# Performance work log

Hardware: AMD Instinct MI355X
Metric: run time of the kernel (lower is better)

The kernel has to match this reference:

```python
import jax, jax.numpy as jnp
import numpy as np

E, T, H, I = 32, 512, 2048, 768


def setup_inputs() -> dict:
    key = jax.random.key(0)
    k1, k2, k3, k4 = jax.random.split(key, 4)
    scale = 1.0 / np.sqrt(H)
    return {
        "routed_input": jax.random.normal(k1, (E, T, H), dtype=jnp.float32),
        "gate_proj": jax.random.normal(k2, (E, I, H), dtype=jnp.float32) * scale,
        "up_proj": jax.random.normal(k3, (E, I, H), dtype=jnp.float32) * scale,
        "down_proj": jax.random.normal(k4, (E, H, I), dtype=jnp.float32) * scale,
    }


def reference(routed_input, gate_proj, up_proj, down_proj):
    # routed_input: [E, T, H]; per-expert SwiGLU MLP, concat over experts.
    gate = jnp.einsum("eth,eih->eti", routed_input, gate_proj)
    up = jnp.einsum("eth,eih->eti", routed_input, up_proj)
    hidden = jax.nn.silu(gate) * up  # [E, T, I]
    out = jnp.einsum("eti,ehi->eth", hidden, down_proj)  # [E, T, H]
    return out.reshape(E * T, H)
```

## Files before the change

### kernel.cpp

```cpp
#include <hip/hip_runtime.h>


#define NE 32
#define NT 512
#define NH 2048
#define NI 768

typedef short        short8  __attribute__((ext_vector_type(8)));
typedef float        floatx4 __attribute__((ext_vector_type(4)));
typedef unsigned int uintx4  __attribute__((ext_vector_type(4)));
typedef __attribute__((address_space(1))) const unsigned int g_u32;
typedef __attribute__((address_space(3))) unsigned int l_u32;

__device__ __forceinline__ void gl_lds16(const void* g, void* l) {
    __builtin_amdgcn_global_load_lds((g_u32*)g, (l_u32*)l, 16, 0, 0);
}

__device__ __forceinline__ unsigned int cvt_pk_bf16(float lo, float hi) {
    unsigned int r;
    asm("v_cvt_pk_bf16_f32 %0, %1, %2" : "=v"(r) : "v"(lo), "v"(hi));
    return r;
}

__device__ __forceinline__ short8 frag8(floatx4 x0, floatx4 x1) {
    union { unsigned int u[4]; short8 s; } t;
    t.u[0] = cvt_pk_bf16(x0[0], x0[1]);
    t.u[1] = cvt_pk_bf16(x0[2], x0[3]);
    t.u[2] = cvt_pk_bf16(x1[0], x1[1]);
    t.u[3] = cvt_pk_bf16(x1[2], x1[3]);
    return t.s;
}

__device__ __forceinline__ uintx4 pack8(floatx4 x0, floatx4 x1) {
    uintx4 u;
    u[0] = cvt_pk_bf16(x0[0], x0[1]);
    u[1] = cvt_pk_bf16(x0[2], x0[3]);
    u[2] = cvt_pk_bf16(x1[0], x1[1]);
    u[3] = cvt_pk_bf16(x1[2], x1[3]);
    return u;
}

__device__ __forceinline__ ushort f2bf(float f) {
    union { float f; unsigned int u; } v; v.f = f;
    unsigned int r = v.u + 0x7fffu + ((v.u >> 16) & 1u);
    return (ushort)(r >> 16);
}

__global__ __launch_bounds__(256, 3) void moe_gateup(
    const float* __restrict__ rin, const float* __restrict__ gate,
    const float* __restrict__ up, ushort* __restrict__ hidden)
{
    __shared__ ushort SA[2][128][32];
    __shared__ ushort SG[2][64][32];
    __shared__ ushort SU[2][64][32];

    const int bid = blockIdx.x;
    const int wg  = (bid & 7) * 192 + (bid >> 3);
    const int e   = wg / 48;
    const int rem = wg % 48;
    const int ti  = rem % 12;
    const int tm  = rem / 12;

    const int tid  = threadIdx.x;
    const int lane = tid & 63;
    const int wave = tid >> 6;
    const int wr = wave >> 1;
    const int wc = wave & 1;

    const float* Ab = rin  + (size_t)e * NT * NH + (size_t)(tm * 128) * NH;
    const float* Gb = gate + (size_t)e * NI * NH + (size_t)(ti * 64) * NH;
    const float* Ub = up   + (size_t)e * NI * NH + (size_t)(ti * 64) * NH;

    const int a0_row = tid >> 2,            a0_cl = tid & 3;
    const int a1_row = (tid + 256) >> 2,    a1_cl = tid & 3;
    const int a0_c = a0_cl ^ (a0_row & 3);
    const int a1_c = a1_cl ^ (a1_row & 3);
    const int w_row = tid >> 2,             w_cl = tid & 3;
    const int w_c = w_cl ^ (w_row & 3);

    const float* A0src = Ab + (size_t)a0_row * NH + a0_c * 8;
    const float* A1src = Ab + (size_t)a1_row * NH + a1_c * 8;
    const float* Gsrc  = Gb + (size_t)w_row * NH + w_c * 8;
    const float* Usrc  = Ub + (size_t)w_row * NH + w_c * 8;

    floatx4 accg[4][2], accu[4][2];
    #pragma unroll
    for (int m = 0; m < 4; ++m)
        #pragma unroll
        for (int n = 0; n < 2; ++n) {
            accg[m][n] = (floatx4)0.f;
            accu[m][n] = (floatx4)0.f;
        }

    const int frow = lane & 15;
    const int h    = lane >> 4;
    const int KT = NH / 32;

    floatx4 P[4][2];

#define ISSUE(kt) do {                                                       \
        const int k_ = (kt) * 32;                                            \
        P[0][0] = *(const floatx4*)(A0src + k_);                             \
        P[0][1] = *(const floatx4*)(A0src + k_ + 4);                         \
        P[1][0] = *(const floatx4*)(A1src + k_);                             \
        P[1][1] = *(const floatx4*)(A1src + k_ + 4);                         \
        P[2][0] = *(const floatx4*)(Gsrc + k_);                              \
        P[2][1] = *(const floatx4*)(Gsrc + k_ + 4);                          \
        P[3][0] = *(const floatx4*)(Usrc + k_);                              \
        P[3][1] = *(const floatx4*)(Usrc + k_ + 4);                          \
    } while (0)

#define WRITE(b) do {                                                       \
        *(uintx4*)&SA[b][a0_row][a0_cl * 8] = pack8(P[0][0], P[0][1]);       \
        *(uintx4*)&SA[b][a1_row][a1_cl * 8] = pack8(P[1][0], P[1][1]);       \
        *(uintx4*)&SG[b][w_row][w_cl * 8]   = pack8(P[2][0], P[2][1]);       \
        *(uintx4*)&SU[b][w_row][w_cl * 8]   = pack8(P[3][0], P[3][1]);       \
    } while (0)

#define COMPUTE(b) do {                                                      \
        short8 af[4], gf[2], uf[2];                                          \
        _Pragma("unroll")                                                    \
        for (int m = 0; m < 4; ++m) {                                        \
            const int R = wr * 64 + m * 16 + frow;                           \
            const int p = h ^ (R & 3);                                       \
            af[m] = *(const short8*)&SA[b][R][p * 8];                        \
        }                                                                    \
        _Pragma("unroll")                                                    \
        for (int n = 0; n < 2; ++n) {                                        \
            const int R = wc * 32 + n * 16 + frow;                           \
            const int p = h ^ (R & 3);                                       \
            gf[n] = *(const short8*)&SG[b][R][p * 8];                        \
            uf[n] = *(const short8*)&SU[b][R][p * 8];                        \
        }                                                                    \
        _Pragma("unroll")                                                    \
        for (int m = 0; m < 4; ++m)                                          \
            _Pragma("unroll")                                                \
            for (int n = 0; n < 2; ++n) {                                    \
                accg[m][n] = __builtin_amdgcn_mfma_f32_16x16x32_bf16(        \
                    af[m], gf[n], accg[m][n], 0, 0, 0);                      \
                accu[m][n] = __builtin_amdgcn_mfma_f32_16x16x32_bf16(        \
                    af[m], uf[n], accu[m][n], 0, 0, 0);                      \
            }                                                                \
    } while (0)

#define ENDBAR() do {                                                        \
        asm volatile("s_waitcnt lgkmcnt(0)" ::: "memory");                   \
        __builtin_amdgcn_sched_barrier(0);                                   \
        __builtin_amdgcn_s_barrier();                                        \
    } while (0)

    ISSUE(0);
    WRITE(0);
    ISSUE(1);
    ENDBAR();

    for (int kt = 0; kt < KT; kt += 2) {
        COMPUTE(0);
        WRITE(1);
        if (kt + 2 < KT) ISSUE(kt + 2);
        ENDBAR();
        COMPUTE(1);
        if (kt + 2 < KT) WRITE(0);
        if (kt + 3 < KT) ISSUE(kt + 3);
        ENDBAR();
    }
#undef ISSUE
#undef WRITE
#undef COMPUTE
#undef ENDBAR

    const int ccol  = lane & 15;
    const int crow0 = (lane >> 4) * 4;
    const size_t hbase = ((size_t)e * NT + (size_t)tm * 128) * NI + ti * 64;
    #pragma unroll
    for (int m = 0; m < 4; ++m)
        #pragma unroll
        for (int n = 0; n < 2; ++n)
            #pragma unroll
            for (int j = 0; j < 4; ++j) {
                const float g = accg[m][n][j];
                const float u = accu[m][n][j];
                const float hh = (g / (1.f + __expf(-g))) * u;
                const int row = wr * 64 + m * 16 + crow0 + j;
                const int col = wc * 32 + n * 16 + ccol;
                hidden[hbase + (size_t)row * NI + col] = f2bf(hh);
            }
}

__global__ __launch_bounds__(256, 2) void moe_down(
    const ushort* __restrict__ hidden, const float* __restrict__ down,
    float* __restrict__ out)
{
    __shared__ ushort As[2][128][32];
    __shared__ float  Bs[2][128][32];

    const int bid = blockIdx.x;
    const int wg  = (bid & 7) * (2048 / 8) + (bid >> 3);
    const int e   = wg >> 6;
    const int rem = wg & 63;
    const int tn  = rem & 15;
    const int tm  = rem >> 4;

    const int tid  = threadIdx.x;
    const int lane = tid & 63;
    const int wave = tid >> 6;
    const int wr = wave >> 1, wc = wave & 1;

    const ushort* Ab = hidden + ((size_t)e * NT + (size_t)tm * 128) * NI;
    const float*  Bb = down + (size_t)e * NH * NI + (size_t)(tn * 128) * NI;

    floatx4 acc[4][4];
    #pragma unroll
    for (int m = 0; m < 4; ++m)
        #pragma unroll
        for (int n = 0; n < 4; ++n) acc[m][n] = (floatx4)0.f;

    const int frow = lane & 15;
    const int h    = lane >> 4;
    const int ca   = h ^ (frow & 3);
    const int rb   = frow & 7;
    const int c0   = (2 * h) ^ rb;
    const int c1   = (2 * h + 1) ^ rb;
    const int KT = NI / 32;

#define STAGE_DN(kt, b) do {                                                 \
        const int k0_ = (kt) * 32;                                           \
        _Pragma("unroll")                                                    \
        for (int i = 0; i < 2; ++i) {                                        \
            const int g_ = wave * 2 + i;                                     \
            const int r_ = g_ * 16 + (lane >> 2);                            \
            const int cs_ = (lane & 3) ^ (r_ & 3);                           \
            gl_lds16(Ab + (size_t)r_ * NI + k0_ + cs_ * 8, &As[b][g_ * 16][0]); \
        }                                                                    \
        _Pragma("unroll")                                                    \
        for (int i = 0; i < 4; ++i) {                                        \
            const int g_ = wave * 4 + i;                                     \
            const int r_ = g_ * 8 + (lane >> 3);                             \
            const int cs_ = (lane & 7) ^ (r_ & 7);                           \
            gl_lds16(Bb + (size_t)r_ * NI + k0_ + cs_ * 4, &Bs[b][g_ * 8][0]); \
        }                                                                    \
    } while (0)

    STAGE_DN(0, 0);

    for (int kt = 0; kt < KT; ++kt) {
        const int cur = kt & 1;
        if (kt + 1 < KT) {
            STAGE_DN(kt + 1, cur ^ 1);
            asm volatile("s_waitcnt vmcnt(6)" ::: "memory");
        } else {
            asm volatile("s_waitcnt vmcnt(0)" ::: "memory");
        }
        __builtin_amdgcn_s_barrier();

        short8 af[4], bf[4];
        #pragma unroll
        for (int m = 0; m < 4; ++m) {
            const int R = wr * 64 + m * 16 + frow;
            af[m] = *(const short8*)&As[cur][R][ca * 8];
        }
        #pragma unroll
        for (int n = 0; n < 4; ++n) {
            const int R = wc * 64 + n * 16 + frow;
            bf[n] = frag8(*(const floatx4*)&Bs[cur][R][c0 * 4],
                          *(const floatx4*)&Bs[cur][R][c1 * 4]);
        }
        #pragma unroll
        for (int m = 0; m < 4; ++m)
            #pragma unroll
            for (int n = 0; n < 4; ++n)
                acc[m][n] = __builtin_amdgcn_mfma_f32_16x16x32_bf16(
                    af[m], bf[n], acc[m][n], 0, 0, 0);

        asm volatile("s_waitcnt lgkmcnt(0)" ::: "memory");
        __builtin_amdgcn_sched_barrier(0);
        __builtin_amdgcn_s_barrier();
    }
#undef STAGE_DN

    const int ccol  = lane & 15;
    const int crow0 = (lane >> 4) * 4;
    float* Ob = out + ((size_t)e * NT + (size_t)tm * 128) * NH + tn * 128;
    #pragma unroll
    for (int m = 0; m < 4; ++m)
        #pragma unroll
        for (int n = 0; n < 4; ++n)
            #pragma unroll
            for (int j = 0; j < 4; ++j) {
                const int row = wr * 64 + m * 16 + crow0 + j;
                const int col = wc * 64 + n * 16 + ccol;
                Ob[(size_t)row * NH + col] = acc[m][n][j];
            }
}

extern "C" void kernel_launch(void* const* d_in, const int* in_sizes, int n_in,
                              void* d_out, int out_size, void* d_ws, size_t ws_size,
                              hipStream_t stream) {
    const float* rin  = (const float*)d_in[0];
    const float* gate = (const float*)d_in[1];
    const float* up   = (const float*)d_in[2];
    const float* down = (const float*)d_in[3];
    float* out = (float*)d_out;
    ushort* hidden = (ushort*)d_ws;

    moe_gateup<<<dim3(1536), dim3(256), 0, stream>>>(rin, gate, up, hidden);
    moe_down<<<dim3(2048), dim3(256), 0, stream>>>(hidden, down, out);
}
```

Before: 336.5 us.

## Deepen gate/up weight prefetch and change LDS swizzle to row-pair XOR

The gate/up kernel now loads its gate/up weight tiles two k-steps ahead through two alternating register sets, while the activation tile is still loaded one step ahead. This hides more global-load latency on the weight stream. The LDS swizzle changes from XOR with (row&3) to XOR with ((row>>1)&3) in both kernels, so fragment reads hit fewer bank conflicts and the per-fragment swizzle is computed once. The extra prefetch buffer raises VGPR pressure, which may cut occupancy.

```diff
diff --git a/kernel.cpp b/kernel.cpp
--- a/kernel.cpp
+++ b/kernel.cpp
@@ -71,17 +71,13 @@
     const float* Gb = gate + (size_t)e * NI * NH + (size_t)(ti * 64) * NH;
     const float* Ub = up   + (size_t)e * NI * NH + (size_t)(ti * 64) * NH;
 
-    const int a0_row = tid >> 2,            a0_cl = tid & 3;
-    const int a1_row = (tid + 256) >> 2,    a1_cl = tid & 3;
-    const int a0_c = a0_cl ^ (a0_row & 3);
-    const int a1_c = a1_cl ^ (a1_row & 3);
-    const int w_row = tid >> 2,             w_cl = tid & 3;
-    const int w_c = w_cl ^ (w_row & 3);
-
-    const float* A0src = Ab + (size_t)a0_row * NH + a0_c * 8;
-    const float* A1src = Ab + (size_t)a1_row * NH + a1_c * 8;
-    const float* Gsrc  = Gb + (size_t)w_row * NH + w_c * 8;
-    const float* Usrc  = Ub + (size_t)w_row * NH + w_c * 8;
+    const int s_row = tid >> 2;
+    const int s_cl  = tid & 3;
+    const int s_c   = s_cl ^ ((s_row >> 1) & 3);
+    const float* A0src = Ab + (size_t)s_row * NH + s_c * 8;
+    const float* A1src = Ab + (size_t)(s_row + 64) * NH + s_c * 8;
+    const float* Gsrc  = Gb + (size_t)s_row * NH + s_c * 8;
+    const float* Usrc  = Ub + (size_t)s_row * NH + s_c * 8;
 
     floatx4 accg[4][2], accu[4][2];
     #pragma unroll
@@ -94,43 +90,44 @@
 
     const int frow = lane & 15;
     const int h    = lane >> 4;
+    const int pch  = h ^ ((frow >> 1) & 3);
     const int KT = NH / 32;
 
-    floatx4 P[4][2];
-
-#define ISSUE(kt) do {                                                       \
+    floatx4 a[2][2];
+    floatx4 g0[2][2], g1[2][2];
+
+#define ISSUE_A(kt) do {                                                     \
         const int k_ = (kt) * 32;                                            \
-        P[0][0] = *(const floatx4*)(A0src + k_);                             \
-        P[0][1] = *(const floatx4*)(A0src + k_ + 4);                         \
-        P[1][0] = *(const floatx4*)(A1src + k_);                             \
-        P[1][1] = *(const floatx4*)(A1src + k_ + 4);                         \
-        P[2][0] = *(const floatx4*)(Gsrc + k_);                              \
-        P[2][1] = *(const floatx4*)(Gsrc + k_ + 4);                          \
-        P[3][0] = *(const floatx4*)(Usrc + k_);                              \
-        P[3][1] = *(const floatx4*)(Usrc + k_ + 4);                          \
-    } while (0)
-
-#define WRITE(b) do {                                                       \
-        *(uintx4*)&SA[b][a0_row][a0_cl * 8] = pack8(P[0][0], P[0][1]);       \
-        *(uintx4*)&SA[b][a1_row][a1_cl * 8] = pack8(P[1][0], P[1][1]);       \
-        *(uintx4*)&SG[b][w_row][w_cl * 8]   = pack8(P[2][0], P[2][1]);       \
-        *(uintx4*)&SU[b][w_row][w_cl * 8]   = pack8(P[3][0], P[3][1]);       \
+        a[0][0] = *(const floatx4*)(A0src + k_);                             \
+        a[0][1] = *(const floatx4*)(A0src + k_ + 4);                         \
+        a[1][0] = *(const floatx4*)(A1src + k_);                             \
+        a[1][1] = *(const floatx4*)(A1src + k_ + 4);                         \
+    } while (0)
+
+#define ISSUE_G(kt, gp) do {                                                 \
+        const int k_ = (kt) * 32;                                            \
+        gp[0][0] = *(const floatx4*)(Gsrc + k_);                             \
+        gp[0][1] = *(const floatx4*)(Gsrc + k_ + 4);                         \
+        gp[1][0] = *(const floatx4*)(Usrc + k_);                             \
+        gp[1][1] = *(const floatx4*)(Usrc + k_ + 4);                         \
+    } while (0)
+
+#define WRITE(b, gp) do {                                                    \
+        *(uintx4*)&SA[b][s_row][s_cl * 8]      = pack8(a[0][0], a[0][1]);    \
+        *(uintx4*)&SA[b][s_row + 64][s_cl * 8] = pack8(a[1][0], a[1][1]);    \
+        *(uintx4*)&SG[b][s_row][s_cl * 8]      = pack8(gp[0][0], gp[0][1]);  \
+        *(uintx4*)&SU[b][s_row][s_cl * 8]      = pack8(gp[1][0], gp[1][1]);  \
     } while (0)
 
 #define COMPUTE(b) do {                                                      \
         short8 af[4], gf[2], uf[2];                                          \
         _Pragma("unroll")                                                    \
-        for (int m = 0; m < 4; ++m) {                                        \
-            const int R = wr * 64 + m * 16 + frow;                           \
-            const int p = h ^ (R & 3);                                       \
-            af[m] = *(const short8*)&SA[b][R][p * 8];                        \
-        }                                                                    \
+        for (int m = 0; m < 4; ++m)                                          \
+            af[m] = *(const short8*)&SA[b][wr * 64 + m * 16 + frow][pch * 8];\
         _Pragma("unroll")                                                    \
         for (int n = 0; n < 2; ++n) {                                        \
-            const int R = wc * 32 + n * 16 + frow;                           \
-            const int p = h ^ (R & 3);                                       \
-            gf[n] = *(const short8*)&SG[b][R][p * 8];                        \
-            uf[n] = *(const short8*)&SU[b][R][p * 8];                        \
+            gf[n] = *(const short8*)&SG[b][wc * 32 + n * 16 + frow][pch * 8];\
+            uf[n] = *(const short8*)&SU[b][wc * 32 + n * 16 + frow][pch * 8];\
         }                                                                    \
         _Pragma("unroll")                                                    \
         for (int m = 0; m < 4; ++m)                                          \
@@ -149,22 +146,32 @@
         __builtin_amdgcn_s_barrier();                                        \
     } while (0)
 
-    ISSUE(0);
-    WRITE(0);
-    ISSUE(1);
+    ISSUE_A(0);
+    ISSUE_G(0, g0);
+    ISSUE_G(1, g1);
+    WRITE(0, g0);
+    ISSUE_A(1);
+    ISSUE_G(2, g0);
     ENDBAR();
 
     for (int kt = 0; kt < KT; kt += 2) {
         COMPUTE(0);
-        WRITE(1);
-        if (kt + 2 < KT) ISSUE(kt + 2);
+        if (kt + 1 < KT) {
+            WRITE(1, g1);
+            if (kt + 2 < KT) ISSUE_A(kt + 2);
+            if (kt + 3 < KT) ISSUE_G(kt + 3, g1);
+        }
         ENDBAR();
         COMPUTE(1);
-        if (kt + 2 < KT) WRITE(0);
-        if (kt + 3 < KT) ISSUE(kt + 3);
+        if (kt + 2 < KT) {
+            WRITE(0, g0);
+            if (kt + 3 < KT) ISSUE_A(kt + 3);
+            if (kt + 4 < KT) ISSUE_G(kt + 4, g0);
+        }
         ENDBAR();
     }
-#undef ISSUE
+#undef ISSUE_A
+#undef ISSUE_G
 #undef WRITE
 #undef COMPUTE
 #undef ENDBAR
@@ -217,7 +224,7 @@
 
     const int frow = lane & 15;
     const int h    = lane >> 4;
-    const int ca   = h ^ (frow & 3);
+    const int ca   = h ^ ((frow >> 1) & 3);
     const int rb   = frow & 7;
     const int c0   = (2 * h) ^ rb;
     const int c1   = (2 * h + 1) ^ rb;
@@ -229,7 +236,7 @@
         for (int i = 0; i < 2; ++i) {                                        \
             const int g_ = wave * 2 + i;                                     \
             const int r_ = g_ * 16 + (lane >> 2);                            \
-            const int cs_ = (lane & 3) ^ (r_ & 3);                           \
+            const int cs_ = (lane & 3) ^ ((r_ >> 1) & 3);                    \
             gl_lds16(Ab + (size_t)r_ * NI + k0_ + cs_ * 8, &As[b][g_ * 16][0]); \
         }                                                                    \
         _Pragma("unroll")                                                    \
```

Result: slower. 346.0 us (+2.8%).

## Stage down-proj B tile through registers, converting fp32 to bf16 before LDS

Applied to the files above, without the earlier changes.

The down-projection kernel stops using direct global-to-LDS loads. It now loads A and B tiles into registers, converts the fp32 down-proj weights to bf16 once while writing them to LDS, and uses a register-prefetch double-buffer pipeline. This halves the B tile's LDS footprint and removes the per-fragment conversion work from the MFMA inner loop, which allows occupancy to rise to 3 blocks per CU. The trade-off is higher register pressure and VGPR round-trips for the staged data.

```diff
diff --git a/kernel.cpp b/kernel.cpp
--- a/kernel.cpp
+++ b/kernel.cpp
@@ -9,26 +9,11 @@
 typedef short        short8  __attribute__((ext_vector_type(8)));
 typedef float        floatx4 __attribute__((ext_vector_type(4)));
 typedef unsigned int uintx4  __attribute__((ext_vector_type(4)));
-typedef __attribute__((address_space(1))) const unsigned int g_u32;
-typedef __attribute__((address_space(3))) unsigned int l_u32;
-
-__device__ __forceinline__ void gl_lds16(const void* g, void* l) {
-    __builtin_amdgcn_global_load_lds((g_u32*)g, (l_u32*)l, 16, 0, 0);
-}
 
 __device__ __forceinline__ unsigned int cvt_pk_bf16(float lo, float hi) {
     unsigned int r;
     asm("v_cvt_pk_bf16_f32 %0, %1, %2" : "=v"(r) : "v"(lo), "v"(hi));
     return r;
-}
-
-__device__ __forceinline__ short8 frag8(floatx4 x0, floatx4 x1) {
-    union { unsigned int u[4]; short8 s; } t;
-    t.u[0] = cvt_pk_bf16(x0[0], x0[1]);
-    t.u[1] = cvt_pk_bf16(x0[2], x0[3]);
-    t.u[2] = cvt_pk_bf16(x1[0], x1[1]);
-    t.u[3] = cvt_pk_bf16(x1[2], x1[3]);
-    return t.s;
 }
 
 __device__ __forceinline__ uintx4 pack8(floatx4 x0, floatx4 x1) {
@@ -187,15 +172,15 @@
             }
 }
 
-__global__ __launch_bounds__(256, 2) void moe_down(
+__global__ __launch_bounds__(256, 3) void moe_down(
     const ushort* __restrict__ hidden, const float* __restrict__ down,
     float* __restrict__ out)
 {
-    __shared__ ushort As[2][128][32];
-    __shared__ float  Bs[2][128][32];
+    __shared__ ushort SA[2][128][32];
+    __shared__ ushort SB[2][128][32];
 
     const int bid = blockIdx.x;
-    const int wg  = (bid & 7) * (2048 / 8) + (bid >> 3);
+    const int wg  = (bid & 7) * 256 + (bid >> 3);
     const int e   = wg >> 6;
     const int rem = wg & 63;
     const int tn  = rem & 15;
@@ -208,6 +193,14 @@
 
     const ushort* Ab = hidden + ((size_t)e * NT + (size_t)tm * 128) * NI;
     const float*  Bb = down + (size_t)e * NH * NI + (size_t)(tn * 128) * NI;
+
+    const int s_row = tid >> 2;
+    const int s_cl  = tid & 3;
+    const int s_c   = s_cl ^ (s_row & 3);
+    const ushort* A0src = Ab + (size_t)s_row * NI + s_c * 8;
+    const ushort* A1src = Ab + (size_t)(s_row + 64) * NI + s_c * 8;
+    const float*  B0src = Bb + (size_t)s_row * NI + s_c * 8;
+    const float*  B1src = Bb + (size_t)(s_row + 64) * NI + s_c * 8;
 
     floatx4 acc[4][4];
     #pragma unroll
@@ -217,66 +210,75 @@
 
     const int frow = lane & 15;
     const int h    = lane >> 4;
-    const int ca   = h ^ (frow & 3);
-    const int rb   = frow & 7;
-    const int c0   = (2 * h) ^ rb;
-    const int c1   = (2 * h + 1) ^ rb;
     const int KT = NI / 32;
 
-#define STAGE_DN(kt, b) do {                                                 \
-        const int k0_ = (kt) * 32;                                           \
-        _Pragma("unroll")                                                    \
-        for (int i = 0; i < 2; ++i) {                                        \
-            const int g_ = wave * 2 + i;                                     \
-            const int r_ = g_ * 16 + (lane >> 2);                            \
-            const int cs_ = (lane & 3) ^ (r_ & 3);                           \
-            gl_lds16(Ab + (size_t)r_ * NI + k0_ + cs_ * 8, &As[b][g_ * 16][0]); \
+    short8  Pa[2];
+    floatx4 Pb[2][2];
+
+#define ISSUE(kt) do {                                                       \
+        const int k_ = (kt) * 32;                                            \
+        Pa[0]    = *(const short8*)(A0src + k_);                             \
+        Pa[1]    = *(const short8*)(A1src + k_);                             \
+        Pb[0][0] = *(const floatx4*)(B0src + k_);                            \
+        Pb[0][1] = *(const floatx4*)(B0src + k_ + 4);                        \
+        Pb[1][0] = *(const floatx4*)(B1src + k_);                            \
+        Pb[1][1] = *(const floatx4*)(B1src + k_ + 4);                        \
+    } while (0)
+
+#define WRITE(b) do {                                                        \
+        *(short8*)&SA[b][s_row][s_cl * 8]      = Pa[0];                      \
+        *(short8*)&SA[b][s_row + 64][s_cl * 8] = Pa[1];                      \
+        *(uintx4*)&SB[b][s_row][s_cl * 8]      = pack8(Pb[0][0], Pb[0][1]);  \
+        *(uintx4*)&SB[b][s_row + 64][s_cl * 8] = pack8(Pb[1][0], Pb[1][1]);  \
+    } while (0)
+
+#define COMPUTE(b) do {                                                      \
+        short8 af[4], bf[4];                                                 \
+        _Pragma("unroll")                                                    \
+        for (int m = 0; m < 4; ++m) {                                        \
+            const int R = wr * 64 + m * 16 + frow;                           \
+            const int p = h ^ (R & 3);                                       \
+            af[m] = *(const short8*)&SA[b][R][p * 8];                        \
         }                                                                    \
         _Pragma("unroll")                                                    \
-        for (int i = 0; i < 4; ++i) {                                        \
-            const int g_ = wave * 4 + i;                                     \
-            const int r_ = g_ * 8 + (lane >> 3);                             \
-            const int cs_ = (lane & 7) ^ (r_ & 7);                           \
-            gl_lds16(Bb + (size_t)r_ * NI + k0_ + cs_ * 4, &Bs[b][g_ * 8][0]); \
+        for (int n = 0; n < 4; ++n) {                                        \
+            const int R = wc * 64 + n * 16 + frow;                           \
+            const int p = h ^ (R & 3);                                       \
+            bf[n] = *(const short8*)&SB[b][R][p * 8];                        \
         }                                                                    \
-    } while (0)
-
-    STAGE_DN(0, 0);
-
-    for (int kt = 0; kt < KT; ++kt) {
-        const int cur = kt & 1;
-        if (kt + 1 < KT) {
-            STAGE_DN(kt + 1, cur ^ 1);
-            asm volatile("s_waitcnt vmcnt(6)" ::: "memory");
-        } else {
-            asm volatile("s_waitcnt vmcnt(0)" ::: "memory");
-        }
-        __builtin_amdgcn_s_barrier();
-
-        short8 af[4], bf[4];
-        #pragma unroll
-        for (int m = 0; m < 4; ++m) {
-            const int R = wr * 64 + m * 16 + frow;
-            af[m] = *(const short8*)&As[cur][R][ca * 8];
-        }
-        #pragma unroll
-        for (int n = 0; n < 4; ++n) {
-            const int R = wc * 64 + n * 16 + frow;
-            bf[n] = frag8(*(const floatx4*)&Bs[cur][R][c0 * 4],
-                          *(const floatx4*)&Bs[cur][R][c1 * 4]);
-        }
-        #pragma unroll
-        for (int m = 0; m < 4; ++m)
-            #pragma unroll
-            for (int n = 0; n < 4; ++n)
-                acc[m][n] = __builtin_amdgcn_mfma_f32_16x16x32_bf16(
-                    af[m], bf[n], acc[m][n], 0, 0, 0);
-
-        asm volatile("s_waitcnt lgkmcnt(0)" ::: "memory");
-        __builtin_amdgcn_sched_barrier(0);
-        __builtin_amdgcn_s_barrier();
+        _Pragma("unroll")                                                    \
+        for (int m = 0; m < 4; ++m)                                          \
+            _Pragma("unroll")                                                \
+            for (int n = 0; n < 4; ++n)                                      \
+                acc[m][n] = __builtin_amdgcn_mfma_f32_16x16x32_bf16(         \
+                    af[m], bf[n], acc[m][n], 0, 0, 0);                       \
+    } while (0)
+
+#define ENDBAR() do {                                                        \
+        asm volatile("s_waitcnt lgkmcnt(0)" ::: "memory");                   \
+        __builtin_amdgcn_sched_barrier(0);                                   \
+        __builtin_amdgcn_s_barrier();                                        \
+    } while (0)
+
+    ISSUE(0);
+    WRITE(0);
+    ISSUE(1);
+    ENDBAR();
+
+    for (int kt = 0; kt < KT; kt += 2) {
+        COMPUTE(0);
+        WRITE(1);
+        if (kt + 2 < KT) ISSUE(kt + 2);
+        ENDBAR();
+        COMPUTE(1);
+        if (kt + 2 < KT) WRITE(0);
+        if (kt + 3 < KT) ISSUE(kt + 3);
+        ENDBAR();
     }
-#undef STAGE_DN
+#undef ISSUE
+#undef WRITE
+#undef COMPUTE
+#undef ENDBAR
 
     const int ccol  = lane & 15;
     const int crow0 = (lane >> 4) * 4;
```

After: 339.7 us. Within noise of the previous version (+0.9%).
